# Optimization experiments

Hardware: AMD Instinct MI355X
Metric: run time of the kernel (lower is better)

Reference implementation:

```python
import jax, jax.numpy as jnp
import numpy as np

B, D, H, E, K = 8192, 1024, 4096, 8, 2
LOSS_COEF = 0.01
EPS_COMBINE = float(np.finfo(np.float64).eps)  # np.finfo(float).eps used in combine


def setup_inputs() -> dict:
    key = jax.random.key(0)
    ks = jax.random.split(key, 6)
    s_in = 1.0 / np.sqrt(D)
    s_hid = 1.0 / np.sqrt(H)
    return {
        "x": jax.random.normal(ks[0], (B, D), jnp.float32),
        "w_gate": jax.random.uniform(ks[1], (E, D), jnp.float32, -s_in, s_in),
        "fc1_w": jax.random.uniform(ks[2], (E, H, D), jnp.float32, -s_in, s_in),
        "fc1_b": jax.random.uniform(ks[3], (E, H), jnp.float32, -s_in, s_in),
        "fc2_w": jax.random.uniform(ks[4], (E, D, H), jnp.float32, -s_hid, s_hid),
        "fc2_b": jax.random.uniform(ks[5], (E, D), jnp.float32, -s_hid, s_hid),
    }


def _cv_squared(v):
    # torch .var() uses ddof=1
    return jnp.var(v, ddof=1) / (jnp.mean(v) ** 2 + 1e-10)


def _top_k_gating(x, w_gate):
    # clean logits (noisy_gating=False): [B, E]
    logits = x @ w_gate.T
    top_vals, top_idx = jax.lax.top_k(logits, K + 1)  # min(k+1, E)
    topk_vals = top_vals[:, :K]
    topk_idx = top_idx[:, :K]
    topk_gates = jax.nn.softmax(topk_vals, axis=1)
    gates = jnp.zeros((x.shape[0], E), x.dtype)
    gates = gates.at[jnp.arange(x.shape[0])[:, None], topk_idx].set(topk_gates)
    return gates


def _forward(x, w_gate, fc1_w, fc1_b, fc2_w, fc2_b):
    gates = _top_k_gating(x, w_gate)            # [B, E], sparse (k nonzeros/row)
    importance = gates.sum(axis=0)              # [E]
    load = (gates > 0).sum(axis=0).astype(jnp.float32)
    loss = (_cv_squared(importance) + _cv_squared(load)) * LOSS_COEF

    # Dense-equivalent expert compute: tokens with gate==0 contribute 0 to the
    # combine, identical math to SparseDispatcher's gather/scatter.
    h = jnp.einsum('bd,ehd->beh', x, fc1_w) + fc1_b            # [B, E, H]
    h = jax.nn.gelu(h, approximate=False)                      # torch exact gelu
    o = jnp.einsum('beh,edh->bed', h, fc2_w) + fc2_b           # [B, E, D]
    log_p = jax.nn.log_softmax(o, axis=-1)                     # LogSoftmax(dim=1)

    # combine: exp, weight by gates, scatter-add, eps-fill, log
    combined = jnp.einsum('be,bed->bd', gates, jnp.exp(log_p)) # [B, D]
    combined = jnp.where(combined == 0, EPS_COMBINE, combined)
    y = jnp.log(combined)
    return y, loss


def reference(x, w_gate, fc1_w, fc1_b, fc2_w, fc2_b):
    return _forward(x, w_gate, fc1_w, fc1_b, fc2_w, fc2_b)
```

## Files before the change

### kernel.cpp

```cpp
#include <hip/hip_runtime.h>
#include <cstdint>
#include <cmath>

#define BT 8192
#define DD 1024
#define HH 4096
#define EE 8
#define MT2 72

typedef __attribute__((ext_vector_type(8))) short short8;
typedef __attribute__((ext_vector_type(4))) float f32x4;
typedef unsigned short u16;
typedef unsigned int u32;

__device__ __forceinline__ u16 f2bf(float f) {
    u32 u = __float_as_uint(f);
    u += 0x7FFFu + ((u >> 16) & 1u);
    return (u16)(u >> 16);
}

__device__ __forceinline__ void gld_lds16(const void* g, void* l) {
    __builtin_amdgcn_global_load_lds((__attribute__((address_space(1))) void*)g,
                                     (__attribute__((address_space(3))) void*)l,
                                     16, 0, 0);
}

__global__ void cvt_kernel(const float* __restrict__ src, u16* __restrict__ dst, int n8) {
    int i = blockIdx.x * blockDim.x + threadIdx.x;
    if (i >= n8) return;
    size_t base = (size_t)i * 8;
    float4 a = *(const float4*)(src + base);
    float4 b = *(const float4*)(src + base + 4);
    uint4 o;
    o.x = (u32)f2bf(a.x) | ((u32)f2bf(a.y) << 16);
    o.y = (u32)f2bf(a.z) | ((u32)f2bf(a.w) << 16);
    o.z = (u32)f2bf(b.x) | ((u32)f2bf(b.y) << 16);
    o.w = (u32)f2bf(b.z) | ((u32)f2bf(b.w) << 16);
    *(uint4*)(dst + base) = o;
}

__global__ void gating_kernel(const float* __restrict__ x, const float* __restrict__ wg,
                              float* __restrict__ gate_arr, int* __restrict__ list,
                              int* __restrict__ info,
                              int* __restrict__ counts, float* __restrict__ importance) {
    int wave = (blockIdx.x * blockDim.x + threadIdx.x) >> 6;
    int lane = threadIdx.x & 63;
    if (wave >= BT) return;
    const float* xr = x + (size_t)wave * DD;
    double acc[EE];
#pragma unroll
    for (int e = 0; e < EE; ++e) acc[e] = 0.0;
#pragma unroll
    for (int c = 0; c < DD / 256; ++c) {
        const int i = c * 256 + lane * 4;
        float4 xv = *(const float4*)(xr + i);
        double x0 = xv.x, x1 = xv.y, x2 = xv.z, x3 = xv.w;
#pragma unroll
        for (int e = 0; e < EE; ++e) {
            float4 wv = *(const float4*)(wg + e * DD + i);
            acc[e] += x0 * (double)wv.x + x1 * (double)wv.y
                    + x2 * (double)wv.z + x3 * (double)wv.w;
        }
    }
#pragma unroll
    for (int e = 0; e < EE; ++e) {
        double v = acc[e];
        for (int off = 32; off; off >>= 1) v += __shfl_down(v, off, 64);
        acc[e] = v;
    }
    if (lane == 0) {
        int i0 = 0; double v0 = acc[0];
        for (int e = 1; e < EE; ++e) if (acc[e] > v0) { v0 = acc[e]; i0 = e; }
        int i1 = -1; double v1 = -1e300;
        for (int e = 0; e < EE; ++e) { if (e == i0) continue; if (acc[e] > v1) { v1 = acc[e]; i1 = e; } }
        double e1 = exp(v1 - v0);
        double s = 1.0 + e1;
        float g0 = (float)(1.0 / s);
        float g1 = (float)(e1 / s);
        gate_arr[2 * wave]     = g0;
        gate_arr[2 * wave + 1] = g1;
        atomicAdd(&importance[i0], g0);
        atomicAdd(&importance[i1], g1);
        int p0 = atomicAdd(&counts[i0], 1);
        list[i0 * BT + p0] = wave;
        int p1 = atomicAdd(&counts[i1], 1);
        list[i1 * BT + p1] = wave;
        info[2 * wave]     = (i0 << 16) | p0;
        info[2 * wave + 1] = (i1 << 16) | p1;
    }
}

__global__ void loss_kernel(const int* __restrict__ counts, const float* __restrict__ importance,
                            int* __restrict__ offs, float* __restrict__ out_loss,
                            int* __restrict__ tmap, int* __restrict__ ntiles) {
    if (threadIdx.x == 0 && blockIdx.x == 0) {
        double mi = 0, ml = 0;
        int off = 0;
        for (int e = 0; e < EE; e++) {
            offs[e] = off; off += counts[e];
            mi += (double)importance[e]; ml += (double)counts[e];
        }
        mi /= EE; ml /= EE;
        double vi = 0, vl = 0;
        for (int e = 0; e < EE; e++) {
            double di = (double)importance[e] - mi; vi += di * di;
            double dl = (double)counts[e] - ml;     vl += dl * dl;
        }
        vi /= (EE - 1); vl /= (EE - 1);
        double cv_i = vi / (mi * mi + 1e-10);
        double cv_l = vl / (ml * ml + 1e-10);
        *out_loss = (float)((cv_i + cv_l) * 0.01);
        int ntl = 0;
        for (int e = 0; e < EE; e++)
            for (int t = 0; t < counts[e]; t += 256)
                tmap[ntl++] = (e << 20) | t;
        *ntiles = ntl;
    }
}

__global__ void gather_x_kernel(const float* __restrict__ x, const int* __restrict__ list,
                                const int* __restrict__ counts, const int* __restrict__ offs,
                                u16* __restrict__ xg) {
    int r = blockIdx.x;
    int e = 0;
#pragma unroll
    for (int i = 1; i < EE; ++i) if (r >= offs[i]) e = i;
    int m = r - offs[e];
    if (m >= counts[e]) return;
    int token = list[e * BT + m];
    const float* src = x + (size_t)token * DD;
    u16* dst = xg + (size_t)r * DD;
    int i = threadIdx.x * 4;
    float4 a = *(const float4*)(src + i);
    uint2 o;
    o.x = (u32)f2bf(a.x) | ((u32)f2bf(a.y) << 16);
    o.y = (u32)f2bf(a.z) | ((u32)f2bf(a.w) << 16);
    *(uint2*)(dst + i) = o;
}

template <int K, int NT, bool GELU, bool GATHER>
__global__ __launch_bounds__(512) void moe_gemm(const u16* __restrict__ Asrc,
                                                const u16* __restrict__ Bsrc,
                                                const float* __restrict__ bias,
                                                const int* __restrict__ list,
                                                const int* __restrict__ counts,
                                                const int* __restrict__ offs,
                                                const int* __restrict__ tmap,
                                                const int* __restrict__ ntiles,
                                                u16* __restrict__ outB,
                                                float* __restrict__ outF) {
    constexpr int NXT = NT / 256;
    constexpr int nwg = NXT * MT2;
    constexpr int q = nwg / 8;
    const int bid = blockIdx.x;
    const int wg = (bid & 7) * q + (bid >> 3);
    const int nt = wg / MT2;
    const int mt = wg - nt * MT2;
    if (mt >= *ntiles) return;
    const int ent = tmap[mt];
    const int e = ent >> 20;
    const int mbase = ent & 0xFFFFF;
    const int cnt = counts[e];
    const int mmax = cnt - mbase;
    const int rowbase = offs[e] + mbase;
    const int nbase = nt * 256;
    const int tid = threadIdx.x;
    const int lane = tid & 63;
    const int wv = tid >> 6;

    __shared__ u16 As0[256 * 32], As1[256 * 32];
    __shared__ u16 Bs0[256 * 32], Bs1[256 * 32];
    __shared__ int rows_lds[256];

    if constexpr (GATHER) {
        if (tid < 256) {
            int m = min(tid, mmax - 1);
            rows_lds[tid] = list[e * BT + mbase + m];
        }
        __syncthreads();
    }

    const int myrow = tid & 255;
    const int kch = tid >> 8;
    size_t arow;
    if constexpr (GATHER) arow = (size_t)rows_lds[myrow];
    else                  arow = (size_t)(rowbase + min(myrow, mmax - 1));
    const u16* aptr = Asrc + arow * (size_t)K + kch * 8;
    const u16* bptr = Bsrc + ((size_t)e * NT + nbase + myrow) * (size_t)K + kch * 8;

    f32x4 acc[8][4] = {};
    const int moff = (wv >> 2) * 128;
    const int noff = (wv & 3) * 64;
    const int kq = lane >> 4;
    const int rsub = lane & 15;

#define STAGE(Ad, Bd, k0)                                              \
    do {                                                               \
        gld_lds16(aptr + (k0),      &(Ad)[(kch * 256 + myrow) * 8]);   \
        gld_lds16(aptr + (k0) + 16, &(Ad)[((kch + 2) * 256 + myrow) * 8]); \
        gld_lds16(bptr + (k0),      &(Bd)[(kch * 256 + myrow) * 8]);   \
        gld_lds16(bptr + (k0) + 16, &(Bd)[((kch + 2) * 256 + myrow) * 8]); \
    } while (0)

#define COMPUTE(Ad, Bd)                                                              \
    do {                                                                             \
        short8 af[8], bfr[4];                                                        \
        _Pragma("unroll")                                                            \
        for (int mi = 0; mi < 8; mi++)                                               \
            af[mi] = *(const short8*)&(Ad)[(kq * 256 + moff + mi * 16 + rsub) * 8];  \
        _Pragma("unroll")                                                            \
        for (int ni = 0; ni < 4; ni++)                                               \
            bfr[ni] = *(const short8*)&(Bd)[(kq * 256 + noff + ni * 16 + rsub) * 8]; \
        _Pragma("unroll")                                                            \
        for (int mi = 0; mi < 8; mi++)                                               \
            _Pragma("unroll")                                                        \
            for (int ni = 0; ni < 4; ni++)                                           \
                acc[mi][ni] = __builtin_amdgcn_mfma_f32_16x16x32_bf16(                \
                    af[mi], bfr[ni], acc[mi][ni], 0, 0, 0);                          \
    } while (0)

    STAGE(As0, Bs0, 0);
    __syncthreads();
    for (int k0 = 0; k0 < K; k0 += 64) {
        STAGE(As1, Bs1, k0 + 32);
        COMPUTE(As0, Bs0);
        __syncthreads();
        if (k0 + 64 < K) STAGE(As0, Bs0, k0 + 64);
        COMPUTE(As1, Bs1);
        __syncthreads();
    }
#undef STAGE
#undef COMPUTE

    const int rq = (lane >> 4) * 4;
    float bvals[4];
#pragma unroll
    for (int ni = 0; ni < 4; ni++)
        bvals[ni] = bias[(size_t)e * NT + nbase + noff + ni * 16 + rsub];
#pragma unroll
    for (int mi = 0; mi < 8; mi++) {
#pragma unroll
        for (int r = 0; r < 4; r++) {
            int m = moff + mi * 16 + rq + r;
            if (m < mmax) {
                size_t ro = (size_t)(rowbase + m);
#pragma unroll
                for (int ni = 0; ni < 4; ni++) {
                    int n = nbase + noff + ni * 16 + rsub;
                    float v = acc[mi][ni][r] + bvals[ni];
                    if constexpr (GELU) {
                        v = 0.5f * v * (1.0f + erff(v * 0.7071067811865476f));
                        outB[ro * NT + n] = f2bf(v);
                    } else {
                        outF[ro * NT + n] = v;
                    }
                }
            }
        }
    }
}

__global__ void combine_kernel(const float* __restrict__ o, const float* __restrict__ gates,
                               const int* __restrict__ info, const int* __restrict__ offs,
                               float* __restrict__ y) {
    const int b = blockIdx.x;
    const int tid = threadIdx.x;
    const int lane = tid & 63, wv = tid >> 6;
    const int inf0 = info[2 * b], inf1 = info[2 * b + 1];
    const int r0i = offs[inf0 >> 16] + (inf0 & 0xffff);
    const int r1i = offs[inf1 >> 16] + (inf1 & 0xffff);
    const float* r0 = o + (size_t)r0i * DD;
    const float* r1 = o + (size_t)r1i * DD;
    float v0[4], v1[4];
#pragma unroll
    for (int j = 0; j < 4; j++) { v0[j] = r0[tid + 256 * j]; v1[j] = r1[tid + 256 * j]; }
    float m0 = fmaxf(fmaxf(v0[0], v0[1]), fmaxf(v0[2], v0[3]));
    float m1 = fmaxf(fmaxf(v1[0], v1[1]), fmaxf(v1[2], v1[3]));
#pragma unroll
    for (int off = 32; off; off >>= 1) {
        m0 = fmaxf(m0, __shfl_xor(m0, off, 64));
        m1 = fmaxf(m1, __shfl_xor(m1, off, 64));
    }
    __shared__ float sred[2][4];
    if (lane == 0) { sred[0][wv] = m0; sred[1][wv] = m1; }
    __syncthreads();
    m0 = fmaxf(fmaxf(sred[0][0], sred[0][1]), fmaxf(sred[0][2], sred[0][3]));
    m1 = fmaxf(fmaxf(sred[1][0], sred[1][1]), fmaxf(sred[1][2], sred[1][3]));
    float p0[4], p1[4], s0 = 0.f, s1 = 0.f;
#pragma unroll
    for (int j = 0; j < 4; j++) {
        p0[j] = expf(v0[j] - m0); s0 += p0[j];
        p1[j] = expf(v1[j] - m1); s1 += p1[j];
    }
#pragma unroll
    for (int off = 32; off; off >>= 1) {
        s0 += __shfl_xor(s0, off, 64);
        s1 += __shfl_xor(s1, off, 64);
    }
    __shared__ float sred2[2][4];
    if (lane == 0) { sred2[0][wv] = s0; sred2[1][wv] = s1; }
    __syncthreads();
    s0 = sred2[0][0] + sred2[0][1] + sred2[0][2] + sred2[0][3];
    s1 = sred2[1][0] + sred2[1][1] + sred2[1][2] + sred2[1][3];
    const float c0 = gates[2 * b] / s0;
    const float c1 = gates[2 * b + 1] / s1;
#pragma unroll
    for (int j = 0; j < 4; j++) {
        float c = p0[j] * c0 + p1[j] * c1;
        if (c == 0.f) c = 2.2204460492503131e-16f;
        y[(size_t)b * DD + tid + 256 * j] = logf(c);
    }
}

extern "C" void kernel_launch(void* const* d_in, const int* in_sizes, int n_in,
                              void* d_out, int out_size, void* d_ws, size_t ws_size,
                              hipStream_t stream) {
    const float* x     = (const float*)d_in[0];
    const float* wgate = (const float*)d_in[1];
    const float* fc1w  = (const float*)d_in[2];
    const float* fc1b  = (const float*)d_in[3];
    const float* fc2w  = (const float*)d_in[4];
    const float* fc2b  = (const float*)d_in[5];
    float* out = (float*)d_out;

    char* ws = (char*)d_ws;
    const size_t MB = 1024 * 1024;
    const bool big = ws_size >= 289 * MB;
    u16* w1b = (u16*)(ws);
    float* o = (float*)(ws);
    u16* w2b = (u16*)(ws + 64 * MB);
    u16* xb  = (u16*)(ws + 128 * MB);
    u16* h   = (u16*)(ws + (big ? 128 : 144) * MB);
    u16* xg  = (u16*)(ws + 256 * MB);
    char* meta = ws + (big ? 288 : 272) * MB;
    int* counts       = (int*)meta;
    int* offs         = (int*)(meta + 32);
    float* importance = (float*)(meta + 64);
    int* ntiles       = (int*)(meta + 96);
    float* gate_arr   = (float*)(meta + 128);
    int* info         = (int*)(meta + 128 + 65536);
    int* list         = (int*)(meta + 128 + 131072);
    int* tmap         = (int*)(meta + 512 * 1024);

    hipMemsetAsync(meta, 0, 96, stream);
    cvt_kernel<<<(EE * HH * DD / 8 + 255) / 256, 256, 0, stream>>>(fc1w, w1b, EE * HH * DD / 8);
    cvt_kernel<<<(EE * DD * HH / 8 + 255) / 256, 256, 0, stream>>>(fc2w, w2b, EE * DD * HH / 8);
    gating_kernel<<<BT / 4, 256, 0, stream>>>(x, wgate, gate_arr, list, info, counts, importance);
    loss_kernel<<<1, 64, 0, stream>>>(counts, importance, offs, out + (size_t)BT * DD, tmap, ntiles);

    if (big) {
        gather_x_kernel<<<2 * BT, 256, 0, stream>>>(x, list, counts, offs, xg);
        moe_gemm<DD, HH, true, false><<<(HH / 256) * MT2, 512, 0, stream>>>(
            xg, w1b, fc1b, nullptr, counts, offs, tmap, ntiles, h, nullptr);
    } else {
        cvt_kernel<<<(BT * DD / 8 + 255) / 256, 256, 0, stream>>>(x, xb, BT * DD / 8);
        moe_gemm<DD, HH, true, true><<<(HH / 256) * MT2, 512, 0, stream>>>(
            xb, w1b, fc1b, list, counts, offs, tmap, ntiles, h, nullptr);
    }
    moe_gemm<HH, DD, false, false><<<(DD / 256) * MT2, 512, 0, stream>>>(
        h, w2b, fc2b, nullptr, counts, offs, tmap, ntiles, nullptr, o);
    combine_kernel<<<BT, 256, 0, stream>>>(o, gate_arr, info, offs, out);
}
```

Before: 1.308 ms.

## Restructure MoE GEMM into persistent 8-phase ping-pong pipeline with finer LDS staging

The grouped MoE GEMM becomes a persistent kernel launched with 256 workgroups that loop over tiles. Each 256x256 tile is split into four 128x128 quadrants that run as eight phases per K-step of 128. Global-to-LDS loads are interleaved between phases, with explicit vmcnt waits, raw s_barrier calls and s_setprio around the MFMA bursts. The goal is to hide load latency and barrier stalls behind MFMA work and to cut launch and tail overhead. In exchange the code leans on hand-tuned waitcnt ordering, which is fragile, and a 256-workgroup grid may leave load imbalance across the remaining tiles.

```diff
diff --git a/kernel.cpp b/kernel.cpp
--- a/kernel.cpp
+++ b/kernel.cpp
@@ -151,113 +151,161 @@
                                                 float* __restrict__ outF) {
     constexpr int NXT = NT / 256;
     constexpr int nwg = NXT * MT2;
-    constexpr int q = nwg / 8;
-    const int bid = blockIdx.x;
-    const int wg = (bid & 7) * q + (bid >> 3);
-    const int nt = wg / MT2;
-    const int mt = wg - nt * MT2;
-    if (mt >= *ntiles) return;
-    const int ent = tmap[mt];
-    const int e = ent >> 20;
-    const int mbase = ent & 0xFFFFF;
-    const int cnt = counts[e];
-    const int mmax = cnt - mbase;
-    const int rowbase = offs[e] + mbase;
-    const int nbase = nt * 256;
+    constexpr int QW = nwg / 8;
+    constexpr int ITERS = K / 128;
     const int tid = threadIdx.x;
     const int lane = tid & 63;
     const int wv = tid >> 6;
-
-    __shared__ u16 As0[256 * 32], As1[256 * 32];
-    __shared__ u16 Bs0[256 * 32], Bs1[256 * 32];
-    __shared__ int rows_lds[256];
-
-    if constexpr (GATHER) {
-        if (tid < 256) {
-            int m = min(tid, mmax - 1);
-            rows_lds[tid] = list[e * BT + mbase + m];
-        }
-        __syncthreads();
-    }
-
-    const int myrow = tid & 255;
-    const int kch = tid >> 8;
-    size_t arow;
-    if constexpr (GATHER) arow = (size_t)rows_lds[myrow];
-    else                  arow = (size_t)(rowbase + min(myrow, mmax - 1));
-    const u16* aptr = Asrc + arow * (size_t)K + kch * 8;
-    const u16* bptr = Bsrc + ((size_t)e * NT + nbase + myrow) * (size_t)K + kch * 8;
-
-    f32x4 acc[8][4] = {};
-    const int moff = (wv >> 2) * 128;
-    const int noff = (wv & 3) * 64;
+    const int wqr = wv >> 2;
+    const int wqc = wv & 3;
     const int kq = lane >> 4;
     const int rsub = lane & 15;
-
-#define STAGE(Ad, Bd, k0)                                              \
-    do {                                                               \
-        gld_lds16(aptr + (k0),      &(Ad)[(kch * 256 + myrow) * 8]);   \
-        gld_lds16(aptr + (k0) + 16, &(Ad)[((kch + 2) * 256 + myrow) * 8]); \
-        gld_lds16(bptr + (k0),      &(Bd)[(kch * 256 + myrow) * 8]);   \
-        gld_lds16(bptr + (k0) + 16, &(Bd)[((kch + 2) * 256 + myrow) * 8]); \
+    const int rq = kq * 4;
+    const int ks1 = tid >> 7;
+    const int r128 = tid & 127;
+
+    __shared__ u16 Ls[2][2][2][8192];
+
+    const int nw = *ntiles;
+
+#define STAGE_A(db, h, T)                                                   \
+    do {                                                                    \
+        gld_lds16(aP##h + (T) * 64,      &Ls[db][0][h][tid * 8]);           \
+        gld_lds16(aP##h + (T) * 64 + 32, &Ls[db][0][h][(tid + 512) * 8]);   \
     } while (0)
-
-#define COMPUTE(Ad, Bd)                                                              \
-    do {                                                                             \
-        short8 af[8], bfr[4];                                                        \
-        _Pragma("unroll")                                                            \
-        for (int mi = 0; mi < 8; mi++)                                               \
-            af[mi] = *(const short8*)&(Ad)[(kq * 256 + moff + mi * 16 + rsub) * 8];  \
-        _Pragma("unroll")                                                            \
-        for (int ni = 0; ni < 4; ni++)                                               \
-            bfr[ni] = *(const short8*)&(Bd)[(kq * 256 + noff + ni * 16 + rsub) * 8]; \
-        _Pragma("unroll")                                                            \
-        for (int mi = 0; mi < 8; mi++)                                               \
-            _Pragma("unroll")                                                        \
-            for (int ni = 0; ni < 4; ni++)                                           \
-                acc[mi][ni] = __builtin_amdgcn_mfma_f32_16x16x32_bf16(                \
-                    af[mi], bfr[ni], acc[mi][ni], 0, 0, 0);                          \
+#define STAGE_B(db, h, T)                                                   \
+    do {                                                                    \
+        gld_lds16(bP##h + (T) * 64,      &Ls[db][1][h][tid * 8]);           \
+        gld_lds16(bP##h + (T) * 64 + 32, &Ls[db][1][h][(tid + 512) * 8]);   \
     } while (0)
-
-    STAGE(As0, Bs0, 0);
-    __syncthreads();
-    for (int k0 = 0; k0 < K; k0 += 64) {
-        STAGE(As1, Bs1, k0 + 32);
-        COMPUTE(As0, Bs0);
-        __syncthreads();
-        if (k0 + 64 < K) STAGE(As0, Bs0, k0 + 64);
-        COMPUTE(As1, Bs1);
-        __syncthreads();
-    }
-#undef STAGE
-#undef COMPUTE
-
-    const int rq = (lane >> 4) * 4;
-    float bvals[4];
-#pragma unroll
-    for (int ni = 0; ni < 4; ni++)
-        bvals[ni] = bias[(size_t)e * NT + nbase + noff + ni * 16 + rsub];
-#pragma unroll
-    for (int mi = 0; mi < 8; mi++) {
-#pragma unroll
-        for (int r = 0; r < 4; r++) {
-            int m = moff + mi * 16 + rq + r;
-            if (m < mmax) {
-                size_t ro = (size_t)(rowbase + m);
-#pragma unroll
-                for (int ni = 0; ni < 4; ni++) {
-                    int n = nbase + noff + ni * 16 + rsub;
-                    float v = acc[mi][ni][r] + bvals[ni];
-                    if constexpr (GELU) {
-                        v = 0.5f * v * (1.0f + erff(v * 0.7071067811865476f));
-                        outB[ro * NT + n] = f2bf(v);
-                    } else {
-                        outF[ro * NT + n] = v;
+#define WAIT4 asm volatile("s_waitcnt vmcnt(4)" ::: "memory")
+#define WAIT0 asm volatile("s_waitcnt vmcnt(0)" ::: "memory")
+#define NOOP ((void)0)
+
+#define PH(db, mh, nh, RDA, STG, WT)                                          \
+    do {                                                                      \
+        if (RDA) {                                                            \
+            _Pragma("unroll") for (int kk = 0; kk < 2; kk++)                  \
+            _Pragma("unroll") for (int mi = 0; mi < 4; mi++)                  \
+                afr[mi][kk] = *(const short8*)&Ls[db][0][mh]                  \
+                    [((kk * 4 + kq) * 128 + wqr * 64 + mi * 16 + rsub) * 8];  \
+        }                                                                     \
+        _Pragma("unroll") for (int kk = 0; kk < 2; kk++)                      \
+        _Pragma("unroll") for (int ni = 0; ni < 2; ni++)                      \
+            bfr[ni][kk] = *(const short8*)&Ls[db][1][nh]                      \
+                [((kk * 4 + kq) * 128 + wqc * 32 + ni * 16 + rsub) * 8];      \
+        STG;                                                                  \
+        __builtin_amdgcn_s_barrier();                                         \
+        __builtin_amdgcn_s_setprio(1);                                        \
+        _Pragma("unroll") for (int mi = 0; mi < 4; mi++)                      \
+        _Pragma("unroll") for (int ni = 0; ni < 2; ni++)                      \
+        _Pragma("unroll") for (int kk = 0; kk < 2; kk++)                      \
+            acc[mh][nh][mi][ni] = __builtin_amdgcn_mfma_f32_16x16x32_bf16(    \
+                afr[mi][kk], bfr[ni][kk], acc[mh][nh][mi][ni], 0, 0, 0);      \
+        __builtin_amdgcn_s_setprio(0);                                        \
+        WT;                                                                   \
+        __builtin_amdgcn_s_barrier();                                         \
+    } while (0)
+
+#pragma unroll 1
+    for (int raw = blockIdx.x; raw < nwg; raw += 256) {
+        const int wg = (raw & 7) * QW + (raw >> 3);
+        const int nt = wg / MT2;
+        const int mt = wg - nt * MT2;
+        if (mt >= nw) continue;
+        const int ent = tmap[mt];
+        const int e = ent >> 20;
+        const int mbase = ent & 0xFFFFF;
+        const int mmax = counts[e] - mbase;
+        const int rowbase = offs[e] + mbase;
+        const int nbase = nt * 256;
+
+        size_t arow0, arow1;
+        if constexpr (GATHER) {
+            arow0 = (size_t)list[e * BT + mbase + min(r128, mmax - 1)];
+            arow1 = (size_t)list[e * BT + mbase + min(128 + r128, mmax - 1)];
+        } else {
+            arow0 = (size_t)(rowbase + min(r128, mmax - 1));
+            arow1 = (size_t)(rowbase + min(128 + r128, mmax - 1));
+        }
+        const u16* aP0 = Asrc + arow0 * (size_t)K + ks1 * 8;
+        const u16* aP1 = Asrc + arow1 * (size_t)K + ks1 * 8;
+        const u16* bP0 = Bsrc + ((size_t)e * NT + nbase + r128) * (size_t)K + ks1 * 8;
+        const u16* bP1 = bP0 + (size_t)128 * K;
+
+        f32x4 acc[2][2][4][2] = {};
+        short8 afr[4][2], bfr[2][2];
+
+        STAGE_A(0, 0, 0); STAGE_B(0, 0, 0); STAGE_A(0, 1, 0); STAGE_B(0, 1, 0);
+        STAGE_A(1, 0, 1); STAGE_B(1, 0, 1);
+        WAIT4;
+        __builtin_amdgcn_s_barrier();
+
+#pragma unroll 1
+        for (int it = 0; it < ITERS - 1; ++it) {
+            const int t = 2 * it;
+            PH(0, 0, 0, 1, STAGE_A(1, 1, t + 1), NOOP);
+            PH(0, 0, 1, 0, STAGE_B(1, 1, t + 1), NOOP);
+            PH(0, 1, 0, 1, STAGE_A(0, 0, t + 2), NOOP);
+            PH(0, 1, 1, 0, STAGE_B(0, 0, t + 2), WAIT4);
+            PH(1, 0, 0, 1, STAGE_A(0, 1, t + 2), NOOP);
+            PH(1, 0, 1, 0, STAGE_B(0, 1, t + 2), NOOP);
+            PH(1, 1, 0, 1, STAGE_A(1, 0, t + 3), NOOP);
+            PH(1, 1, 1, 0, STAGE_B(1, 0, t + 3), WAIT4);
+        }
+        {
+            const int t = 2 * (ITERS - 1);
+            PH(0, 0, 0, 1, STAGE_A(1, 1, t + 1), NOOP);
+            PH(0, 0, 1, 0, STAGE_B(1, 1, t + 1), NOOP);
+            PH(0, 1, 0, 1, NOOP, NOOP);
+            PH(0, 1, 1, 0, NOOP, WAIT0);
+            PH(1, 0, 0, 1, NOOP, NOOP);
+            PH(1, 0, 1, 0, NOOP, NOOP);
+            PH(1, 1, 0, 1, NOOP, NOOP);
+            PH(1, 1, 1, 0, NOOP, NOOP);
+        }
+
+        float bvals[2][2];
+#pragma unroll
+        for (int nh = 0; nh < 2; nh++)
+#pragma unroll
+            for (int ni = 0; ni < 2; ni++)
+                bvals[nh][ni] = bias[(size_t)e * NT + nbase + nh * 128 + wqc * 32 + ni * 16 + rsub];
+#pragma unroll
+        for (int mh = 0; mh < 2; mh++) {
+#pragma unroll
+            for (int mi = 0; mi < 4; mi++) {
+#pragma unroll
+                for (int r = 0; r < 4; r++) {
+                    int m = mh * 128 + wqr * 64 + mi * 16 + rq + r;
+                    if (m < mmax) {
+                        size_t ro = (size_t)(rowbase + m);
+#pragma unroll
+                        for (int nh = 0; nh < 2; nh++) {
+#pragma unroll
+                            for (int ni = 0; ni < 2; ni++) {
+                                int n = nbase + nh * 128 + wqc * 32 + ni * 16 + rsub;
+                                float v = acc[mh][nh][mi][ni][r] + bvals[nh][ni];
+                                if constexpr (GELU) {
+                                    v = 0.5f * v * (1.0f + erff(v * 0.7071067811865476f));
+                                    outB[ro * NT + n] = f2bf(v);
+                                } else {
+                                    outF[ro * NT + n] = v;
+                                }
+                            }
+                        }
                     }
                 }
             }
         }
-    }
+        WAIT0;
+    }
+#undef PH
+#undef STAGE_A
+#undef STAGE_B
+#undef WAIT4
+#undef WAIT0
+#undef NOOP
 }
 
 __global__ void combine_kernel(const float* __restrict__ o, const float* __restrict__ gates,
@@ -350,14 +398,14 @@
 
     if (big) {
         gather_x_kernel<<<2 * BT, 256, 0, stream>>>(x, list, counts, offs, xg);
-        moe_gemm<DD, HH, true, false><<<(HH / 256) * MT2, 512, 0, stream>>>(
+        moe_gemm<DD, HH, true, false><<<256, 512, 0, stream>>>(
             xg, w1b, fc1b, nullptr, counts, offs, tmap, ntiles, h, nullptr);
     } else {
         cvt_kernel<<<(BT * DD / 8 + 255) / 256, 256, 0, stream>>>(x, xb, BT * DD / 8);
-        moe_gemm<DD, HH, true, true><<<(HH / 256) * MT2, 512, 0, stream>>>(
+        moe_gemm<DD, HH, true, true><<<256, 512, 0, stream>>>(
             xb, w1b, fc1b, list, counts, offs, tmap, ntiles, h, nullptr);
     }
-    moe_gemm<HH, DD, false, false><<<(DD / 256) * MT2, 512, 0, stream>>>(
+    moe_gemm<HH, DD, false, false><<<256, 512, 0, stream>>>(
         h, w2b, fc2b, nullptr, counts, offs, tmap, ntiles, nullptr, o);
     combine_kernel<<<BT, 256, 0, stream>>>(o, gate_arr, info, offs, out);
 }
```

After: 1.150 ms. 12.1% less time.
